# Kernel optimization log

Hardware: AMD Instinct MI355X
Metric: run time of the kernel (lower is better)

## Reference

```python
import jax, jax.numpy as jnp
import numpy as np

TH = 1.0  # firing threshold (init arg th)


def setup_inputs() -> dict:
    key = jax.random.key(0)
    ks = jax.random.split(key, 5)
    B, T, C = 16, 2048, 256
    hs_pad = jax.random.normal(ks[0], (B, T, C), dtype=jnp.float32)
    hs_mask = jnp.ones((B, 1, T), dtype=bool)  # unused by the math, kept for signature parity
    conv_w = jax.random.normal(ks[1], (C, C, 3), dtype=jnp.float32) * (1.0 / np.sqrt(3.0 * C))
    conv_b = jax.random.normal(ks[2], (C,), dtype=jnp.float32) * 0.01
    lin_w = jax.random.normal(ks[3], (1, C), dtype=jnp.float32) * (1.0 / np.sqrt(C))
    lin_b = jax.random.normal(ks[4], (1,), dtype=jnp.float32) * 0.01
    return {"hs_pad": hs_pad, "hs_mask": hs_mask, "conv_w": conv_w,
            "conv_b": conv_b, "lin_w": lin_w, "lin_b": lin_b}


def _cif(hs_pad, conv_w, conv_b, lin_w, lin_b):
    B, T, C = hs_pad.shape
    # Conv1d(channels, channels, k=3, pad=1) over time
    x = jnp.transpose(hs_pad, (0, 2, 1))  # [B, C, T]
    x = jax.lax.conv_general_dilated(x, conv_w, (1,), [(1, 1)],
                                     dimension_numbers=("NCH", "OIH", "NCH"))
    x = x + conv_b[None, :, None]
    # Linear(C, 1) + sigmoid -> per-frame weight alpha [B, T]
    alpha = jax.nn.sigmoid(jnp.einsum("bct,c->bt", x, lin_w[0]) + lin_b[0])
    loss_pen = alpha.sum()  # sum over batch of per-utt alpha sums (tf=False path)

    def cif_one(a, h):  # a: [T], h: [T, C]
        buf0 = jnp.zeros((T, C), h.dtype)  # worst case: <= T fires
        carry0 = (a[0], a[0] * h[0], jnp.int32(0), buf0)

        def step(carry, inp):
            aa, hacc, idx, buf = carry
            au, hu = inp
            aa_new = aa + au
            fired = aa_new >= TH
            a1 = TH - aa  # == th - (alpha_accum_new - alpha_u)
            h_fire = hacc + a1 * hu
            buf = buf.at[idx].add(jnp.where(fired, h_fire, 0.0))
            aa_next = jnp.where(fired, au - a1, aa_new)
            hacc_next = jnp.where(fired, (au - a1) * hu, hacc + au * hu)
            return (aa_next, hacc_next, idx + fired.astype(jnp.int32), buf), None

        (aa, hacc, idx, buf), _ = jax.lax.scan(step, carry0, (a[1:], h[1:]))
        tail = aa >= TH / 2
        buf = buf.at[idx].add(jnp.where(tail, hacc, 0.0))
        return buf, idx + tail.astype(jnp.int32)

    cs, lengths = jax.vmap(cif_one)(alpha, hs_pad)  # cs: [B, T, C] zero-padded
    return cs, loss_pen, lengths


def reference(hs_pad, hs_mask, conv_w, conv_b, lin_w, lin_b):
    cs, loss_pen, _ = _cif(hs_pad, conv_w, conv_b, lin_w, lin_b)
    # original returns (cs, None, loss_pen.sum()); None omitted
    return cs, loss_pen
```

## Files before the change

### kernel.cpp

```cpp
#include <hip/hip_runtime.h>
#include <math.h>

constexpr int B = 16, T = 2048, C = 256;

typedef float vfloat4 __attribute__((ext_vector_type(4)));

__global__ void w2_kernel(const float* __restrict__ conv_w,
                          const float* __restrict__ conv_b,
                          const float* __restrict__ lin_w,
                          const float* __restrict__ lin_b,
                          float* __restrict__ w2f,
                          float* __restrict__ bias2) {
    int gid  = blockIdx.x * blockDim.x + threadIdx.x;
    int wv   = gid >> 6;
    int lane = gid & 63;
    if (wv > 768) return;
    float s = 0.f;
    if (wv < 768) {
        int i = wv & 255, k = wv >> 8;
#pragma unroll
        for (int m = 0; m < 4; ++m) {
            int o = lane + 64 * m;
            s = fmaf(lin_w[o], conv_w[((size_t)o * C + i) * 3 + k], s);
        }
    } else {
#pragma unroll
        for (int m = 0; m < 4; ++m) {
            int o = lane + 64 * m;
            s = fmaf(lin_w[o], conv_b[o], s);
        }
    }
#pragma unroll
    for (int off = 32; off; off >>= 1) s += __shfl_down(s, off);
    if (lane == 0) {
        if (wv < 768) w2f[wv] = s;
        else          *bias2 = s + lin_b[0];
    }
}

constexpr int FPW = 8;
__global__ void pdot_kernel(const float* __restrict__ h,
                            const float* __restrict__ w2f,
                            float* __restrict__ P0,
                            float* __restrict__ P1,
                            float* __restrict__ P2) {
    int gid  = blockIdx.x * blockDim.x + threadIdx.x;
    int wave = gid >> 6;
    int lane = gid & 63;
    int g    = lane >> 4;
    int il   = lane & 15;

    const float4* w4 = (const float4*)w2f;
    float4 W0[4], W1[4], W2[4];
#pragma unroll
    for (int m = 0; m < 4; ++m) {
        W0[m] = w4[il * 4 + m];
        W1[m] = w4[64 + il * 4 + m];
        W2[m] = w4[128 + il * 4 + m];
    }

    int frame0 = wave * FPW;
#pragma unroll
    for (int chunk = 0; chunk < FPW / 4; ++chunk) {
        int f = frame0 + chunk * 4 + g;
        const float4* hf = (const float4*)(h + (size_t)f * C);
        float s0 = 0.f, s1 = 0.f, s2 = 0.f;
#pragma unroll
        for (int m = 0; m < 4; ++m) {
            float4 hv = hf[il * 4 + m];
            s0 = fmaf(hv.x, W0[m].x, fmaf(hv.y, W0[m].y,
                 fmaf(hv.z, W0[m].z, fmaf(hv.w, W0[m].w, s0))));
            s1 = fmaf(hv.x, W1[m].x, fmaf(hv.y, W1[m].y,
                 fmaf(hv.z, W1[m].z, fmaf(hv.w, W1[m].w, s1))));
            s2 = fmaf(hv.x, W2[m].x, fmaf(hv.y, W2[m].y,
                 fmaf(hv.z, W2[m].z, fmaf(hv.w, W2[m].w, s2))));
        }
#pragma unroll
        for (int off = 8; off; off >>= 1) {
            s0 += __shfl_xor(s0, off, 16);
            s1 += __shfl_xor(s1, off, 16);
            s2 += __shfl_xor(s2, off, 16);
        }
        if (il == 0) { P0[f] = s0; P1[f] = s1; P2[f] = s2; }
    }
}

__global__ void scan_kernel(const float* __restrict__ P0,
                            const float* __restrict__ P1,
                            const float* __restrict__ P2,
                            const float* __restrict__ bias2,
                            float* __restrict__ alpha,
                            int*   __restrict__ F,
                            float* __restrict__ A1,
                            float* __restrict__ REM,
                            int*   __restrict__ Kaux,
                            float* __restrict__ lossP) {
    __shared__ float wsum[4];
    int b    = blockIdx.x;
    int tid  = threadIdx.x;
    int lane = tid & 63, wid = tid >> 6;
    size_t base = (size_t)b * T;
    float bias = *bias2;

    int t0 = tid * 8;
    float a[8];
    float s8 = 0.f;
#pragma unroll
    for (int j = 0; j < 8; ++j) {
        int t = t0 + j;
        size_t bt = base + t;
        float pre = P1[bt] + bias;
        if (t > 0)     pre += P0[bt - 1];
        if (t < T - 1) pre += P2[bt + 1];
        float av = 1.f / (1.f + expf(-pre));
        a[j] = av;
        s8 += av;
    }

    float x = s8;
#pragma unroll
    for (int off = 1; off < 64; off <<= 1) {
        float y = __shfl_up(x, off);
        if (lane >= off) x += y;
    }
    if (lane == 63) wsum[wid] = x;
    __syncthreads();
    float woff = 0.f;
#pragma unroll
    for (int w = 0; w < 4; ++w)
        if (w < wid) woff += wsum[w];
    float Sprev = woff + (x - s8);

    if (tid == 0)
        lossP[b] = wsum[0] + wsum[1] + wsum[2] + wsum[3];

    int*   Fb = F   + base;
    float* Ab = A1  + base;
    float* Rb = REM + base;
#pragma unroll
    for (int j = 0; j < 8; ++j) {
        int t = t0 + j;
        float S  = Sprev + a[j];
        float kp = floorf(Sprev);
        float k  = floorf(S);
        if (k > kp) {
            int ji = (int)kp;
            Fb[ji] = t;
            Ab[ji] = (kp + 1.0f) - Sprev;
            Rb[ji] = S - k;
        }
        alpha[base + t] = a[j];
        Sprev = S;
    }
    if (tid == 255) {
        float K = floorf(Sprev);
        Kaux[2 * b]     = (int)K;
        Kaux[2 * b + 1] = (Sprev - K >= 0.5f) ? 1 : 0;
    }
}

__global__ void gather_kernel(const float* __restrict__ h,
                              const float* __restrict__ alpha,
                              const int*   __restrict__ F,
                              const float* __restrict__ A1,
                              const float* __restrict__ REM,
                              const int*   __restrict__ Kaux,
                              const float* __restrict__ lossP,
                              float* __restrict__ out) {
    int gid  = blockIdx.x * blockDim.x + threadIdx.x;
    int wv   = gid >> 6;
    int lane = gid & 63;
    if (gid == 0) {
        float s = 0.f;
        for (int i = 0; i < B; ++i) s += lossP[i];
        out[(size_t)B * T * C] = s;
    }
    if (wv >= B * T) return;
    int b = wv >> 11;
    int j = wv & (T - 1);
    int K    = Kaux[2 * b];
    int tail = Kaux[2 * b + 1];
    vfloat4* orow = (vfloat4*)(out + ((size_t)b * T + j) * C) + lane;
    if (j > K || (j == K && !tail)) {
        vfloat4 z = {0.f, 0.f, 0.f, 0.f};
        __builtin_nontemporal_store(z, orow);
        return;
    }
    const float*  ab = alpha + (size_t)b * T;
    const float4* hb = (const float4*)(h + (size_t)b * T * C);
    const int*    Fb = F + (size_t)b * T;

    float4 acc;
    int t;
    if (j > 0) {
        int s = Fb[j - 1];
        float r = REM[(size_t)b * T + j - 1];
        float4 hv = hb[(size_t)s * 64 + lane];
        acc = make_float4(r * hv.x, r * hv.y, r * hv.z, r * hv.w);
        t = s + 1;
    } else {
        acc = make_float4(0.f, 0.f, 0.f, 0.f);
        t = 0;
    }
    int mid_end = (j == K) ? T : Fb[j];
    for (; t < mid_end; ++t) {
        float a = ab[t];
        float4 hv = hb[(size_t)t * 64 + lane];
        acc.x = fmaf(a, hv.x, acc.x);
        acc.y = fmaf(a, hv.y, acc.y);
        acc.z = fmaf(a, hv.z, acc.z);
        acc.w = fmaf(a, hv.w, acc.w);
    }
    if (j < K) {
        float a1 = A1[(size_t)b * T + j];
        float4 hv = hb[(size_t)mid_end * 64 + lane];
        acc.x = fmaf(a1, hv.x, acc.x);
        acc.y = fmaf(a1, hv.y, acc.y);
        acc.z = fmaf(a1, hv.z, acc.z);
        acc.w = fmaf(a1, hv.w, acc.w);
    }
    vfloat4 av = {acc.x, acc.y, acc.z, acc.w};
    __builtin_nontemporal_store(av, orow);
}

extern "C" void kernel_launch(void* const* d_in, const int* in_sizes, int n_in,
                              void* d_out, int out_size, void* d_ws, size_t ws_size,
                              hipStream_t stream) {
    const float* h      = (const float*)d_in[0];
    const float* conv_w = (const float*)d_in[2];
    const float* conv_b = (const float*)d_in[3];
    const float* lin_w  = (const float*)d_in[4];
    const float* lin_b  = (const float*)d_in[5];

    float* out = (float*)d_out;

    float* w2f   = (float*)d_ws;
    float* bias2 = w2f + 768;
    float* alpha = w2f + 1024;
    float* P0    = alpha + B * T;
    float* P1    = P0 + B * T;
    float* P2    = P1 + B * T;
    int*   F     = (int*)P0;
    float* A1    = P1;
    float* REM   = P2;
    int*   Kaux  = (int*)(P2 + B * T);
    float* lossP = (float*)(Kaux + 2 * B);

    hipLaunchKernelGGL(w2_kernel, dim3(193), dim3(256), 0, stream,
                       conv_w, conv_b, lin_w, lin_b, w2f, bias2);

    hipLaunchKernelGGL(pdot_kernel, dim3(B * T / (4 * FPW)), dim3(256), 0, stream,
                       h, w2f, P0, P1, P2);

    hipLaunchKernelGGL(scan_kernel, dim3(B), dim3(256), 0, stream,
                       P0, P1, P2, bias2, alpha, F, A1, REM, Kaux, lossP);

    hipLaunchKernelGGL(gather_kernel, dim3(B * T / 4), dim3(256), 0, stream,
                       h, alpha, F, A1, REM, Kaux, lossP, out);
}
```

Baseline: 36.70 us.

## Fuse scan into gather with redundant per-block scan and shared-memory fire tables

```diff
diff --git a/kernel.cpp b/kernel.cpp
--- a/kernel.cpp
+++ b/kernel.cpp
@@ -10,8 +10,10 @@
                           const float* __restrict__ lin_w,
                           const float* __restrict__ lin_b,
                           float* __restrict__ w2f,
-                          float* __restrict__ bias2) {
+                          float* __restrict__ bias2,
+                          float* __restrict__ out) {
     int gid  = blockIdx.x * blockDim.x + threadIdx.x;
+    if (gid == 0) out[(size_t)B * T * C] = 0.f;
     int wv   = gid >> 6;
     int lane = gid & 63;
     if (wv > 768) return;
@@ -85,19 +87,25 @@
     }
 }
 
-__global__ void scan_kernel(const float* __restrict__ P0,
-                            const float* __restrict__ P1,
-                            const float* __restrict__ P2,
-                            const float* __restrict__ bias2,
-                            float* __restrict__ alpha,
-                            int*   __restrict__ F,
-                            float* __restrict__ A1,
-                            float* __restrict__ REM,
-                            int*   __restrict__ Kaux,
-                            float* __restrict__ lossP) {
+constexpr int RPB = 16;
+__global__ __launch_bounds__(256) void gather_scan(
+    const float* __restrict__ h,
+    const float* __restrict__ P0,
+    const float* __restrict__ P1,
+    const float* __restrict__ P2,
+    const float* __restrict__ bias2,
+    float* __restrict__ out)
+{
+    __shared__ float salpha[T];
     __shared__ float wsum[4];
-    int b    = blockIdx.x;
+    __shared__ float sA1[RPB + 1], sREM[RPB + 1];
+    __shared__ int   sF[RPB + 1];
+    __shared__ int   sK, sTail;
+
     int tid  = threadIdx.x;
+    int bid  = blockIdx.x;
+    int b    = bid >> 7;
+    int j0   = (bid & 127) * RPB;
     int lane = tid & 63, wid = tid >> 6;
     size_t base = (size_t)b * T;
     float bias = *bias2;
@@ -115,6 +123,7 @@
         float av = 1.f / (1.f + expf(-pre));
         a[j] = av;
         s8 += av;
+        salpha[t] = av;
     }
 
     float x = s8;
@@ -131,96 +140,76 @@
         if (w < wid) woff += wsum[w];
     float Sprev = woff + (x - s8);
 
-    if (tid == 0)
-        lossP[b] = wsum[0] + wsum[1] + wsum[2] + wsum[3];
-
-    int*   Fb = F   + base;
-    float* Ab = A1  + base;
-    float* Rb = REM + base;
+    if (tid == 0 && (bid & 127) == 0)
+        atomicAdd(&out[(size_t)B * T * C],
+                  wsum[0] + wsum[1] + wsum[2] + wsum[3]);
+
 #pragma unroll
     for (int j = 0; j < 8; ++j) {
-        int t = t0 + j;
         float S  = Sprev + a[j];
         float kp = floorf(Sprev);
         float k  = floorf(S);
         if (k > kp) {
-            int ji = (int)kp;
-            Fb[ji] = t;
-            Ab[ji] = (kp + 1.0f) - Sprev;
-            Rb[ji] = S - k;
-        }
-        alpha[base + t] = a[j];
+            int ji   = (int)kp;
+            int slot = ji - j0 + 1;
+            if (slot >= 0 && slot <= RPB) {
+                sF[slot]   = t0 + j;
+                sA1[slot]  = (kp + 1.0f) - Sprev;
+                sREM[slot] = S - k;
+            }
+        }
         Sprev = S;
     }
     if (tid == 255) {
         float K = floorf(Sprev);
-        Kaux[2 * b]     = (int)K;
-        Kaux[2 * b + 1] = (Sprev - K >= 0.5f) ? 1 : 0;
-    }
-}
-
-__global__ void gather_kernel(const float* __restrict__ h,
-                              const float* __restrict__ alpha,
-                              const int*   __restrict__ F,
-                              const float* __restrict__ A1,
-                              const float* __restrict__ REM,
-                              const int*   __restrict__ Kaux,
-                              const float* __restrict__ lossP,
-                              float* __restrict__ out) {
-    int gid  = blockIdx.x * blockDim.x + threadIdx.x;
-    int wv   = gid >> 6;
-    int lane = gid & 63;
-    if (gid == 0) {
-        float s = 0.f;
-        for (int i = 0; i < B; ++i) s += lossP[i];
-        out[(size_t)B * T * C] = s;
-    }
-    if (wv >= B * T) return;
-    int b = wv >> 11;
-    int j = wv & (T - 1);
-    int K    = Kaux[2 * b];
-    int tail = Kaux[2 * b + 1];
-    vfloat4* orow = (vfloat4*)(out + ((size_t)b * T + j) * C) + lane;
-    if (j > K || (j == K && !tail)) {
-        vfloat4 z = {0.f, 0.f, 0.f, 0.f};
-        __builtin_nontemporal_store(z, orow);
-        return;
-    }
-    const float*  ab = alpha + (size_t)b * T;
-    const float4* hb = (const float4*)(h + (size_t)b * T * C);
-    const int*    Fb = F + (size_t)b * T;
-
-    float4 acc;
-    int t;
-    if (j > 0) {
-        int s = Fb[j - 1];
-        float r = REM[(size_t)b * T + j - 1];
-        float4 hv = hb[(size_t)s * 64 + lane];
-        acc = make_float4(r * hv.x, r * hv.y, r * hv.z, r * hv.w);
-        t = s + 1;
-    } else {
-        acc = make_float4(0.f, 0.f, 0.f, 0.f);
-        t = 0;
-    }
-    int mid_end = (j == K) ? T : Fb[j];
-    for (; t < mid_end; ++t) {
-        float a = ab[t];
-        float4 hv = hb[(size_t)t * 64 + lane];
-        acc.x = fmaf(a, hv.x, acc.x);
-        acc.y = fmaf(a, hv.y, acc.y);
-        acc.z = fmaf(a, hv.z, acc.z);
-        acc.w = fmaf(a, hv.w, acc.w);
-    }
-    if (j < K) {
-        float a1 = A1[(size_t)b * T + j];
-        float4 hv = hb[(size_t)mid_end * 64 + lane];
-        acc.x = fmaf(a1, hv.x, acc.x);
-        acc.y = fmaf(a1, hv.y, acc.y);
-        acc.z = fmaf(a1, hv.z, acc.z);
-        acc.w = fmaf(a1, hv.w, acc.w);
-    }
-    vfloat4 av = {acc.x, acc.y, acc.z, acc.w};
-    __builtin_nontemporal_store(av, orow);
+        sK    = (int)K;
+        sTail = (Sprev - K >= 0.5f) ? 1 : 0;
+    }
+    __syncthreads();
+
+    int K = sK, tail = sTail;
+    const float4* hb = (const float4*)(h + base * C);
+#pragma unroll
+    for (int r = 0; r < 4; ++r) {
+        int j = j0 + wid * 4 + r;
+        vfloat4* orow = (vfloat4*)(out + (base + j) * C) + lane;
+        if (j > K || (j == K && !tail)) {
+            vfloat4 z = {0.f, 0.f, 0.f, 0.f};
+            __builtin_nontemporal_store(z, orow);
+            continue;
+        }
+        float4 acc;
+        int t;
+        if (j > 0) {
+            int s   = sF[j - j0];
+            float rr = sREM[j - j0];
+            float4 hv = hb[(size_t)s * 64 + lane];
+            acc = make_float4(rr * hv.x, rr * hv.y, rr * hv.z, rr * hv.w);
+            t = s + 1;
+        } else {
+            acc = make_float4(0.f, 0.f, 0.f, 0.f);
+            t = 0;
+        }
+        int mid_end = (j == K) ? T : sF[j - j0 + 1];
+        for (; t < mid_end; ++t) {
+            float av = salpha[t];
+            float4 hv = hb[(size_t)t * 64 + lane];
+            acc.x = fmaf(av, hv.x, acc.x);
+            acc.y = fmaf(av, hv.y, acc.y);
+            acc.z = fmaf(av, hv.z, acc.z);
+            acc.w = fmaf(av, hv.w, acc.w);
+        }
+        if (j < K) {
+            float a1 = sA1[j - j0 + 1];
+            float4 hv = hb[(size_t)mid_end * 64 + lane];
+            acc.x = fmaf(a1, hv.x, acc.x);
+            acc.y = fmaf(a1, hv.y, acc.y);
+            acc.z = fmaf(a1, hv.z, acc.z);
+            acc.w = fmaf(a1, hv.w, acc.w);
+        }
+        vfloat4 av4 = {acc.x, acc.y, acc.z, acc.w};
+        __builtin_nontemporal_store(av4, orow);
+    }
 }
 
 extern "C" void kernel_launch(void* const* d_in, const int* in_sizes, int n_in,
@@ -236,25 +225,16 @@
 
     float* w2f   = (float*)d_ws;
     float* bias2 = w2f + 768;
-    float* alpha = w2f + 1024;
-    float* P0    = alpha + B * T;
+    float* P0    = w2f + 1024;
     float* P1    = P0 + B * T;
     float* P2    = P1 + B * T;
-    int*   F     = (int*)P0;
-    float* A1    = P1;
-    float* REM   = P2;
-    int*   Kaux  = (int*)(P2 + B * T);
-    float* lossP = (float*)(Kaux + 2 * B);
 
     hipLaunchKernelGGL(w2_kernel, dim3(193), dim3(256), 0, stream,
-                       conv_w, conv_b, lin_w, lin_b, w2f, bias2);
+                       conv_w, conv_b, lin_w, lin_b, w2f, bias2, out);
 
     hipLaunchKernelGGL(pdot_kernel, dim3(B * T / (4 * FPW)), dim3(256), 0, stream,
                        h, w2f, P0, P1, P2);
 
-    hipLaunchKernelGGL(scan_kernel, dim3(B), dim3(256), 0, stream,
-                       P0, P1, P2, bias2, alpha, F, A1, REM, Kaux, lossP);
-
-    hipLaunchKernelGGL(gather_kernel, dim3(B * T / 4), dim3(256), 0, stream,
-                       h, alpha, F, A1, REM, Kaux, lossP, out);
-}
+    hipLaunchKernelGGL(gather_scan, dim3(B * T / RPB), dim3(256), 0, stream,
+                       h, P0, P1, P2, bias2, out);
+}
```

New measurement: 49.35 us. 1.34x slower.
